# Performance work log

Hardware: AMD Instinct MI355X
Metric: run time of the kernel (lower is better)

The kernel has to match this reference:

```python
import jax, jax.numpy as jnp
import numpy as np

# Module hyperparameters (from init_kwargs)
B, C, T, H, W = 2, 128, 4, 64, 64
NHEADS = 32
SH, SW = 4, 4          # scales: patch size in H and W
GROUPS = C // 4        # GroupNorm groups = dim // 4
EPS = 1e-5


def _rel_index(t_, h_, w_):
    """(N,N) int32 index into the (2T-1)*(2h-1)*(2w-1) relative-position table."""
    tt = np.arange(t_); yy = np.arange(h_); xx = np.arange(w_)
    coords = np.stack(np.meshgrid(tt, yy, xx, indexing='ij'), -1).reshape(-1, 3)  # (N,3)
    rel = coords[:, None, :] - coords[None, :, :]                                 # (N,N,3)
    rel = rel + np.array([t_ - 1, h_ - 1, w_ - 1])
    idx = (rel[..., 0] * (2 * h_ - 1) + rel[..., 1]) * (2 * w_ - 1) + rel[..., 2]
    return idx.astype(np.int32)


def setup_inputs() -> dict:
    key = jax.random.key(0)
    ks = jax.random.split(key, 6)
    h, w = H // SH, W // SW
    table_sz = (2 * T - 1) * (2 * h - 1) * (2 * w - 1)
    inp = {
        "x": jax.random.normal(ks[0], (B, C, T, H, W), jnp.float32),
        "Wq": jax.random.normal(ks[1], (C, C), jnp.float32) / np.sqrt(C).astype(np.float32),
        "Wk": jax.random.normal(ks[2], (C, C), jnp.float32) / np.sqrt(C).astype(np.float32),
        "Wv": jax.random.normal(ks[3], (C, C), jnp.float32) / np.sqrt(C).astype(np.float32),
        "gq_gamma": jnp.ones((C,), jnp.float32), "gq_beta": jnp.zeros((C,), jnp.float32),
        "gk_gamma": jnp.ones((C,), jnp.float32), "gk_beta": jnp.zeros((C,), jnp.float32),
        "gv_gamma": jnp.ones((C,), jnp.float32), "gv_beta": jnp.zeros((C,), jnp.float32),
        "rel_table": jax.random.normal(ks[4], (NHEADS, table_sz), jnp.float32) * 0.02,
        "rel_index": jnp.asarray(_rel_index(T, h, w)),
    }
    return inp


def _group_norm(z, gamma, beta, groups, eps=EPS):
    b, c = z.shape[:2]
    zg = z.reshape(b, groups, c // groups, *z.shape[2:])
    mu = zg.mean(axis=(2, 3, 4, 5), keepdims=True)
    var = jnp.mean(jnp.square(zg - mu), axis=(2, 3, 4, 5), keepdims=True)
    zg = (zg - mu) * jax.lax.rsqrt(var + eps)
    zn = zg.reshape(z.shape)
    return zn * gamma[None, :, None, None, None] + beta[None, :, None, None, None]


def reference(x, Wq, Wk, Wv, gq_gamma, gq_beta, gk_gamma, gk_beta,
              gv_gamma, gv_beta, rel_table, rel_index):
    b, c, t, hh, ww = x.shape
    h, w = hh // SH, ww // SW
    n = t * h * w           # patch tokens
    p = SH * SW             # pixels per patch
    d = c // NHEADS         # head dim

    # 1x1x1 projections (pointwise conv == channel matmul) + GroupNorm
    q = _group_norm(jnp.einsum('bcthw,oc->bothw', x, Wq), gq_gamma, gq_beta, GROUPS)
    k = _group_norm(jnp.einsum('bcthw,oc->bothw', x, Wk), gk_gamma, gk_beta, GROUPS)
    v = _group_norm(jnp.einsum('bcthw,oc->bothw', x, Wv), gv_gamma, gv_beta, GROUPS)

    def to_patches(z):  # (b,c,t,H,W) -> (b,heads,d,N,P)
        z = z.reshape(b, NHEADS, d, t, h, SH, w, SW)
        z = z.transpose(0, 1, 2, 3, 4, 6, 5, 7)
        return z.reshape(b, NHEADS, d, n, p)

    qp = to_patches(q).mean(-1)     # pooled patch queries (b,g,d,N)
    kp = to_patches(k).mean(-1)     # pooled patch keys    (b,g,d,N)
    vp = to_patches(v)              # full-res values      (b,g,d,N,P)

    scale = 1.0 / jnp.sqrt(jnp.float32(d))
    logits = jnp.einsum('bgdn,bgdm->bgnm', qp, kp) * scale
    logits = logits + rel_table[:, rel_index][None]   # relative position bias (1,g,N,N)
    attn = jax.nn.softmax(logits, axis=-1)

    out = jnp.einsum('bgnm,bgdmp->bgdnp', attn, vp)   # (b,g,d,N,P)
    out = out.reshape(b, NHEADS, d, t, h, w, SH, SW).transpose(0, 1, 2, 3, 4, 6, 5, 7)
    out = out.reshape(b, c, t, hh, ww)                # (B,C,T,H,W) after outer permute
    return out
```

## Files before the change

### kernel.cpp

```cpp
#include <hip/hip_runtime.h>
#include <hip/hip_bf16.h>

#define B_ 2
#define C_ 128
#define G_ 32
#define N_ 1024
#define S_ 16384
#define TABLE_ 6727
#define EPS_ 1e-5f
#define LOG2E_ 1.44269504f
#define PSTB_ 64
#define NSTRIP_ 128

typedef __hip_bfloat16 bf16;
typedef __attribute__((ext_vector_type(8))) short short8;
typedef __attribute__((ext_vector_type(4))) float f32x4;

#if __has_builtin(__builtin_amdgcn_exp2f)
#define EXP2(x) __builtin_amdgcn_exp2f(x)
#else
#define EXP2(x) __expf((x) * 0.69314718056f)
#endif

__device__ __forceinline__ float bf2f(bf16 v) { return __bfloat162float(v); }
__device__ __forceinline__ float bits2f(unsigned u) { return __uint_as_float(u); }
__device__ __forceinline__ int dflag(const void* gq) {
  return (((const unsigned*)gq)[0] != 0x3F803F80u) ? 1 : 0;
}
__device__ __forceinline__ float ldcv(const void* p, int i, int fl) {
  return fl ? ((const float*)p)[i] : bf2f(((const bf16*)p)[i]);
}
__device__ __forceinline__ size_t spidx(int ttm, int b, int g) {
  return ((size_t)(((ttm * B_ + b) * G_) + g)) << 7;
}

__global__ __launch_bounds__(256) void proj_kernel(
    const void* __restrict__ x, const void* __restrict__ Wq,
    const void* __restrict__ Wk, const void* __restrict__ Wv,
    const void* __restrict__ gq,
    float* __restrict__ qpart, float* __restrict__ kpart,
    bf16* __restrict__ vpt, float* __restrict__ sp)
{
  __shared__ bf16 xs[128 * 128];
  __shared__ bf16 vs[8192];
  const int tid = threadIdx.x, lane = tid & 63, w = tid >> 6;
  const int s0 = blockIdx.x * 128;
  const int oh = blockIdx.y;
  const int b  = blockIdx.z;
  const int fl = dflag(gq);

  {
    const int s_lo = tid & 15, cb = tid >> 4;
    const size_t gc = (size_t)b * C_ * S_ + (size_t)(cb * 8) * S_ + s0 + s_lo;
#pragma unroll
    for (int i = 0; i < 8; ++i) {
      const int s = i * 16 + s_lo;
      union { short8 v; bf16 h[8]; } u;
      if (fl) {
#pragma unroll
        for (int j = 0; j < 8; ++j)
          u.h[j] = (bf16)((const float*)x)[gc + i * 16 + (size_t)j * S_];
      } else {
#pragma unroll
        for (int j = 0; j < 8; ++j)
          u.h[j] = ((const bf16*)x)[gc + i * 16 + (size_t)j * S_];
      }
      *(short8*)&xs[s * 128 + ((cb ^ (s & 7)) << 3)] = u.v;
    }
  }

  const int ow = oh * 4 + w;
  const int quad = lane >> 4;
  const int om = ow * 16 + (lane & 15);
  const void* const Ws[3] = {Wq, Wk, Wv};
  short8 afr[3][4];
#pragma unroll
  for (int tt = 0; tt < 3; ++tt)
#pragma unroll
    for (int kk = 0; kk < 4; ++kk) {
      const int off = om * 128 + kk * 32 + quad * 8;
      if (fl) {
        const float* wp = (const float*)Ws[tt] + off;
        const float4 a = *(const float4*)wp, bb = *(const float4*)(wp + 4);
        union { short8 s; bf16 h[8]; } u;
        u.h[0] = (bf16)a.x;  u.h[1] = (bf16)a.y;  u.h[2] = (bf16)a.z;  u.h[3] = (bf16)a.w;
        u.h[4] = (bf16)bb.x; u.h[5] = (bf16)bb.y; u.h[6] = (bf16)bb.z; u.h[7] = (bf16)bb.w;
        afr[tt][kk] = u.s;
      } else {
        afr[tt][kk] = *(const short8*)((const bf16*)Ws[tt] + off);
      }
    }
  __syncthreads();

  float ssum[3] = {0.f, 0.f, 0.f}, ssq[3] = {0.f, 0.f, 0.f};
  float psq[4][4] = {}, psk[4][4] = {};
  const int sl = lane & 15;
#pragma unroll
  for (int st = 0; st < 8; ++st) {
    f32x4 acc[3] = {{0,0,0,0},{0,0,0,0},{0,0,0,0}};
    const int srow = st * 16 + sl;
#pragma unroll
    for (int kk = 0; kk < 4; ++kk) {
      const short8 bv = *(const short8*)
          &xs[srow * 128 + ((((kk << 2) | quad) ^ (sl & 7)) << 3)];
      acc[0] = __builtin_amdgcn_mfma_f32_16x16x32_bf16(afr[0][kk], bv, acc[0], 0, 0, 0);
      acc[1] = __builtin_amdgcn_mfma_f32_16x16x32_bf16(afr[1][kk], bv, acc[1], 0, 0, 0);
      acc[2] = __builtin_amdgcn_mfma_f32_16x16x32_bf16(afr[2][kk], bv, acc[2], 0, 0, 0);
    }
    const int pIdx = (st >> 2) * 4 + (sl & 3);
    const int xp = (st & 3) * 4 + (sl >> 2);
#pragma unroll
    for (int r = 0; r < 4; ++r) {
      const float vq = acc[0][r], vk = acc[1][r], vv = acc[2][r];
      ssum[0] += vq; ssq[0] += vq * vq;
      ssum[1] += vk; ssq[1] += vk * vk;
      ssum[2] += vv; ssq[2] += vv * vv;
      float aq = vq + __shfl_xor(vq, 1); aq += __shfl_xor(aq, 2);
      float ak = vk + __shfl_xor(vk, 1); ak += __shfl_xor(ak, 2);
      psq[r][st & 3] += aq;
      psk[r][st & 3] += ak;
      const int o_loc = w * 16 + quad * 4 + r;
      vs[(o_loc * 8 + pIdx) * 16 + xp] = (bf16)vv;
    }
  }

  {
    const int c = sl & 3, wxl = sl >> 2;
    const int t = s0 >> 12;
    const int yy0 = (s0 >> 6) & 63;
    const int hy = yy0 >> 2, rp = (yy0 >> 1) & 1;
    const int nbase = t * 256 + hy * 16;
    const size_t pb = ((size_t)((b * 2 + rp) * C_ + ow * 16 + quad * 4 + c)) * N_ + nbase;
#pragma unroll
    for (int j = 0; j < 4; ++j) {
      float vq = psq[0][j];
      if (c == 1) vq = psq[1][j];
      if (c == 2) vq = psq[2][j];
      if (c == 3) vq = psq[3][j];
      float vk = psk[0][j];
      if (c == 1) vk = psk[1][j];
      if (c == 2) vk = psk[2][j];
      if (c == 3) vk = psk[3][j];
      qpart[pb + j * 4 + wxl] = vq;
      kpart[pb + j * 4 + wxl] = vk;
    }
  }

#pragma unroll
  for (int tt = 0; tt < 3; ++tt) {
#pragma unroll
    for (int off = 1; off < 16; off <<= 1) {
      ssum[tt] += __shfl_xor(ssum[tt], off);
      ssq[tt]  += __shfl_xor(ssq[tt], off);
    }
    if ((lane & 15) == 0) {
      const int grp = ow * 4 + quad;
      sp[spidx(tt * 2 + 0, b, grp) + blockIdx.x] = ssum[tt];
      sp[spidx(tt * 2 + 1, b, grp) + blockIdx.x] = ssq[tt];
    }
  }
  __syncthreads();

  const int rowp0 = (s0 >> 6) & 63;
  const int mIdx0 = (s0 >> 12) * 256 + (rowp0 >> 2) * 16;
  for (int cid = tid; cid < 1024; cid += 256) {
    const int half = cid & 1, run = cid >> 1;
    const int o_loc = run >> 3, pIdx = run & 7;
    const int o = oh * 64 + o_loc;
    const int gg = o >> 2, dd = o & 3;
    const int colv = dd * 16 + (rowp0 & 3) * 4 + pIdx;
    bf16* dst = vpt + ((size_t)(b * G_ + gg) * 64 + colv) * N_ + mIdx0 + half * 8;
    *(short8*)dst = *(const short8*)&vs[run * 16 + half * 8];
  }
}

__global__ __launch_bounds__(256, 4) void attn_kernel(
    const float* __restrict__ qpart, const float* __restrict__ kpart,
    const bf16* __restrict__ vpt, const void* __restrict__ rt,
    const void* __restrict__ gq, const void* __restrict__ bq,
    const void* __restrict__ gk, const void* __restrict__ bk,
    const void* __restrict__ gv, const void* __restrict__ bv,
    const float* __restrict__ sp, void* __restrict__ outv)
{
  const int g = blockIdx.y, b = blockIdx.z;
  const int tid = threadIdx.x, lane = tid & 63, w = tid >> 6;
  const int nw = blockIdx.x * 64;
  const int fl = dflag(gq);
  __shared__ __align__(16) char smem[37816];
  bf16* Vlds = (bf16*)smem;
  bf16* bldm = (bf16*)(smem + 8192);
  bf16* pldw = (bf16*)(smem + 13216) + w * 16 * PSTB_;
  bf16* klds = (bf16*)(smem + 21408);
  float* red = (float*)(smem + 37792);

  const int col = lane & 15, quad = lane >> 4;
  const size_t bg = (size_t)(b * G_ + g);
  const short* vpb = (const short*)vpt + bg * 64 * N_;
  const int vn0 = tid >> 3, kb8 = tid & 7;

  short8 st[2];
#pragma unroll
  for (int i = 0; i < 2; ++i)
    st[i] = *(const short8*)(vpb + (size_t)(i * 32 + vn0) * N_ + 0 * 64 + kb8 * 8);

  if (w < 2) {
#pragma unroll
    for (int j = 0; j < 3; ++j) {
      const float* a = sp + spidx(w + 2 * j, b, g);
      float v = a[lane] + a[lane + 64];
      v += __shfl_xor(v, 1);  v += __shfl_xor(v, 2);  v += __shfl_xor(v, 4);
      v += __shfl_xor(v, 8);  v += __shfl_xor(v, 16); v += __shfl_xor(v, 32);
      if (lane == 0) red[w + 2 * j] = v;
    }
  }

  const int tn = nw >> 8, yb = (nw >> 4) & 15;
  for (int i = tid; i < 2508; i += 256) {
    const int row = i / 33, d = i - row * 33;
    if (d < 31) {
      const int tm = row / 19, dyi = row - tm * 19;
      const int dt = tn - tm + 3;
      const int dy = yb + dyi;
      bldm[row * 33 + d] = (bf16)(ldcv(rt, g * TABLE_ + (dt * 31 + dy) * 31 + d, fl) * LOG2E_);
    }
  }
  __syncthreads();

  const float muq = red[0] * (1.f / 65536.f);
  const float rq = rsqrtf(red[1] * (1.f / 65536.f) - muq * muq + EPS_);
  const float muk = red[2] * (1.f / 65536.f);
  const float rk = rsqrtf(red[3] * (1.f / 65536.f) - muk * muk + EPS_);

  short8 af = {0, 0, 0, 0, 0, 0, 0, 0};
  if (quad < 2) {
    const int n = nw + w * 16 + col;
    union { short8 s; bf16 h[8]; } u;
#pragma unroll
    for (int d = 0; d < 4; ++d) {
      const int c = g * 4 + d;
      const float sq = qpart[((size_t)((b * 2 + 0) * C_ + c)) * N_ + n]
                     + qpart[((size_t)((b * 2 + 1) * C_ + c)) * N_ + n];
      const float qn = (sq * 0.0625f - muq) * rq * ldcv(gq, c, fl) + ldcv(bq, c, fl);
      const float qs = qn * (0.5f * LOG2E_);
      const bf16 qh = (bf16)qs;
      u.h[d] = qh; u.h[4 + d] = (bf16)(qs - bf2f(qh));
    }
    af = u.s;
  }

  {
    float gkv[4], bkv[4];
#pragma unroll
    for (int d = 0; d < 4; ++d) {
      gkv[d] = ldcv(gk, g * 4 + d, fl);
      bkv[d] = ldcv(bk, g * 4 + d, fl);
    }
#pragma unroll
    for (int i = 0; i < 4; ++i) {
      const int n = i * 256 + tid;
      union { short8 s; bf16 h[8]; } u;
#pragma unroll
      for (int d = 0; d < 4; ++d) {
        const int c = g * 4 + d;
        const float sk = kpart[((size_t)((b * 2 + 0) * C_ + c)) * N_ + n]
                       + kpart[((size_t)((b * 2 + 1) * C_ + c)) * N_ + n];
        const float kn = (sk * 0.0625f - muk) * rk * gkv[d] + bkv[d];
        const bf16 kh = (bf16)kn;
        u.h[d] = kh; u.h[4 + d] = (bf16)(kn - bf2f(kh));
      }
      *(short8*)&klds[n * 8] = u.s;
    }
  }
  __syncthreads();

  const short* klds_s = (const short*)klds;
  const short onebits = (short)0x3F80;
  const short8 ones8 = {onebits, onebits, onebits, onebits,
                        onebits, onebits, onebits, onebits};
  f32x4 acco[4] = {{0,0,0,0},{0,0,0,0},{0,0,0,0},{0,0,0,0}};
  f32x4 accs = {0.f, 0.f, 0.f, 0.f};

  ushort4 kv[4], kvn[4];
#pragma unroll
  for (int t = 0; t < 4; ++t)
    kv[t] = *(const ushort4*)(klds_s + ((0 * 4 + t) * 16 + col) * 8 + (quad & 1) * 4);

  for (int ch = 0; ch < 16; ++ch) {
    if (ch > 0) __syncthreads();
#pragma unroll
    for (int i = 0; i < 2; ++i) {
      const int n = i * 32 + vn0;
      *(short8*)&Vlds[n * 64 + ((kb8 ^ (n & 7)) << 3)] = st[i];
    }
    __syncthreads();
    if (ch < 15) {
#pragma unroll
      for (int i = 0; i < 2; ++i)
        st[i] = *(const short8*)(vpb + (size_t)(i * 32 + vn0) * N_ + (ch + 1) * 64 + kb8 * 8);
#pragma unroll
      for (int t = 0; t < 4; ++t)
        kvn[t] = *(const ushort4*)(klds_s + (((ch + 1) * 4 + t) * 16 + col) * 8 + (quad & 1) * 4);
    }
#pragma unroll
    for (int mt4 = 0; mt4 < 4; ++mt4) {
      const int mt = ch * 4 + mt4;
      const int tm = mt >> 4, ym = mt & 15;
      const short8 bf8 = {(short)kv[mt4].x, (short)kv[mt4].y, (short)kv[mt4].z, (short)kv[mt4].w,
                          (short)kv[mt4].x, (short)kv[mt4].y, (short)kv[mt4].z, (short)kv[mt4].w};
      f32x4 acc = {0.f, 0.f, 0.f, 0.f};
      acc = __builtin_amdgcn_mfma_f32_16x16x32_bf16(af, bf8, acc, 0, 0, 0);
      const int bbase = (tm * 19 + (w + 15 - ym)) * 33 + 15 + quad * 4 - col;
#pragma unroll
      for (int r = 0; r < 4; ++r) {
        const float e = EXP2(acc[r] + bf2f(bldm[bbase + r]));
        const int row = quad * 4 + r;
        pldw[row * PSTB_ + (((mt4 * 2 + (col >> 3)) ^ (row & 7)) << 3) + (col & 7)] = (bf16)e;
      }
    }
    __builtin_amdgcn_s_setprio(1);
#pragma unroll
    for (int ks = 0; ks < 2; ++ks) {
      const short8 a2 = *(const short8*)&pldw[col * PSTB_ + (((ks * 4 + quad) ^ (col & 7)) << 3)];
      accs = __builtin_amdgcn_mfma_f32_16x16x32_bf16(a2, ones8, accs, 0, 0, 0);
#pragma unroll
      for (int cc = 0; cc < 4; ++cc) {
        const int n = cc * 16 + col;
        const int kb = ks * 4 + quad;
        const short8 b2 = *(const short8*)&Vlds[n * 64 + ((kb ^ (n & 7)) << 3)];
        acco[cc] = __builtin_amdgcn_mfma_f32_16x16x32_bf16(a2, b2, acco[cc], 0, 0, 0);
      }
    }
    __builtin_amdgcn_s_setprio(0);
    if (ch < 15) {
#pragma unroll
      for (int t = 0; t < 4; ++t) kv[t] = kvn[t];
    }
  }

  __syncthreads();
  const float mu = red[4] * (1.f / 65536.f);
  const float rs = rsqrtf(red[5] * (1.f / 65536.f) - mu * mu + EPS_);
  const int sh = col >> 2, sw = col & 3;
  const size_t obase = (size_t)(b * C_ + g * 4) * S_ + tn * 4096 + (yb + w) * 256;
  if (!fl) {
    bf16* ost = (bf16*)(smem + w * 2048);
#pragma unroll
    for (int cc = 0; cc < 4; ++cc) {
      const int c = g * 4 + cc;
      const float alpha = rs * ldcv(gv, c, fl);
      const float beta = ldcv(bv, c, fl) - mu * alpha;
#pragma unroll
      for (int r = 0; r < 4; ++r) {
        const int xp = quad * 4 + r;
        ost[cc * 256 + sh * 64 + xp * 4 + sw] = (bf16)(alpha * (acco[cc][r] / accs[r]) + beta);
      }
    }
#pragma unroll
    for (int i = 0; i < 2; ++i) {
      const int e = (i * 64 + lane) * 8;
      const int cc = e >> 8, rem = e & 255;
      *(short8*)((bf16*)outv + obase + (size_t)cc * S_ + rem) = *(const short8*)&ost[e];
    }
  } else {
    float* ostf = (float*)smem + w * 1024;
#pragma unroll
    for (int cc = 0; cc < 4; ++cc) {
      const int c = g * 4 + cc;
      const float alpha = rs * ldcv(gv, c, fl);
      const float beta = ldcv(bv, c, fl) - mu * alpha;
#pragma unroll
      for (int r = 0; r < 4; ++r) {
        const int xp = quad * 4 + r;
        ostf[cc * 256 + sh * 64 + xp * 4 + sw] = alpha * (acco[cc][r] / accs[r]) + beta;
      }
    }
#pragma unroll
    for (int i = 0; i < 4; ++i) {
      const int e = (i * 64 + lane) * 4;
      const int cc = e >> 8, rem = e & 255;
      *(float4*)((float*)outv + obase + (size_t)cc * S_ + rem) = *(const float4*)&ostf[e];
    }
  }
}

extern "C" void kernel_launch(void* const* d_in, const int* in_sizes, int n_in,
                              void* d_out, int out_size, void* d_ws, size_t ws_size,
                              hipStream_t stream) {
  (void)in_sizes; (void)n_in; (void)out_size; (void)ws_size;
  const void* x  = d_in[0];
  const void* Wq = d_in[1];
  const void* Wk = d_in[2];
  const void* Wv = d_in[3];
  const void* gq = d_in[4];
  const void* bq = d_in[5];
  const void* gk = d_in[6];
  const void* bk = d_in[7];
  const void* gv = d_in[8];
  const void* bv = d_in[9];
  const void* rel_table = d_in[10];

  bf16*  vpt  = (bf16*)d_ws;
  float* qpart = (float*)(vpt + (size_t)B_ * G_ * 64 * N_);
  float* kpart = qpart + (size_t)B_ * 2 * C_ * N_;
  float* sp    = kpart + (size_t)B_ * 2 * C_ * N_;

  proj_kernel<<<dim3(NSTRIP_, 2, B_), 256, 0, stream>>>(
      x, Wq, Wk, Wv, gq, qpart, kpart, vpt, sp);
  attn_kernel<<<dim3(16, G_, B_), 256, 0, stream>>>(
      qpart, kpart, vpt, rel_table, gq, bq, gk, bk, gv, bv, sp, d_out);
}
```

Measured before the change: 158.8 us.

## Vectorize x loads with register transpose and make q/k partials channel-contiguous

The x staging in proj_kernel now loads 8 contiguous spatial elements per channel as vector loads. It transposes them in registers before writing to LDS, with a new XOR swizzle that the MFMA read side matches. The pooled q/k partial buffers move from channel-major to position-major with channels innermost, so attn_kernel can fetch a head's 4 channels with a single 16-byte load. This targets the uncoalesced scalar global loads in both kernels, at the cost of strided scattered writes of the partials and extra register shuffling.

```diff
diff --git a/kernel.cpp b/kernel.cpp
--- a/kernel.cpp
+++ b/kernel.cpp
@@ -50,22 +50,32 @@
   const int fl = dflag(gq);
 
   {
-    const int s_lo = tid & 15, cb = tid >> 4;
-    const size_t gc = (size_t)b * C_ * S_ + (size_t)(cb * 8) * S_ + s0 + s_lo;
-#pragma unroll
-    for (int i = 0; i < 8; ++i) {
-      const int s = i * 16 + s_lo;
-      union { short8 v; bf16 h[8]; } u;
-      if (fl) {
-#pragma unroll
-        for (int j = 0; j < 8; ++j)
-          u.h[j] = (bf16)((const float*)x)[gc + i * 16 + (size_t)j * S_];
-      } else {
-#pragma unroll
-        for (int j = 0; j < 8; ++j)
-          u.h[j] = ((const bf16*)x)[gc + i * 16 + (size_t)j * S_];
-      }
-      *(short8*)&xs[s * 128 + ((cb ^ (s & 7)) << 3)] = u.v;
+    const int cb = tid >> 4, sb = tid & 15;
+    const size_t gc0 = (size_t)b * C_ * S_ + (size_t)(cb * 8) * S_ + s0 + sb * 8;
+    union U8 { short8 v; ushort h[8]; };
+    U8 in[8];
+    if (fl) {
+#pragma unroll
+      for (int j = 0; j < 8; ++j) {
+        const float* xp = (const float*)x + gc0 + (size_t)j * S_;
+        const float4 a = *(const float4*)xp, b2 = *(const float4*)(xp + 4);
+        union { short8 s; bf16 hh[8]; } u;
+        u.hh[0] = (bf16)a.x;  u.hh[1] = (bf16)a.y;  u.hh[2] = (bf16)a.z;  u.hh[3] = (bf16)a.w;
+        u.hh[4] = (bf16)b2.x; u.hh[5] = (bf16)b2.y; u.hh[6] = (bf16)b2.z; u.hh[7] = (bf16)b2.w;
+        in[j].v = u.s;
+      }
+    } else {
+#pragma unroll
+      for (int j = 0; j < 8; ++j)
+        in[j].v = *(const short8*)((const bf16*)x + gc0 + (size_t)j * S_);
+    }
+#pragma unroll
+    for (int si = 0; si < 8; ++si) {
+      U8 o;
+#pragma unroll
+      for (int i = 0; i < 8; ++i) o.h[i] = in[i].h[si];
+      const int s = sb * 8 + si;
+      *(short8*)&xs[s * 128 + ((cb ^ si ^ (sb & 7)) << 3)] = o.v;
     }
   }
 
@@ -99,10 +109,11 @@
   for (int st = 0; st < 8; ++st) {
     f32x4 acc[3] = {{0,0,0,0},{0,0,0,0},{0,0,0,0}};
     const int srow = st * 16 + sl;
+    const int rxor = (sl & 7) ^ ((st << 1) & 7) ^ (sl >> 3);
 #pragma unroll
     for (int kk = 0; kk < 4; ++kk) {
       const short8 bv = *(const short8*)
-          &xs[srow * 128 + ((((kk << 2) | quad) ^ (sl & 7)) << 3)];
+          &xs[srow * 128 + ((((kk << 2) | quad) ^ rxor) << 3)];
       acc[0] = __builtin_amdgcn_mfma_f32_16x16x32_bf16(afr[0][kk], bv, acc[0], 0, 0, 0);
       acc[1] = __builtin_amdgcn_mfma_f32_16x16x32_bf16(afr[1][kk], bv, acc[1], 0, 0, 0);
       acc[2] = __builtin_amdgcn_mfma_f32_16x16x32_bf16(afr[2][kk], bv, acc[2], 0, 0, 0);
@@ -130,7 +141,7 @@
     const int yy0 = (s0 >> 6) & 63;
     const int hy = yy0 >> 2, rp = (yy0 >> 1) & 1;
     const int nbase = t * 256 + hy * 16;
-    const size_t pb = ((size_t)((b * 2 + rp) * C_ + ow * 16 + quad * 4 + c)) * N_ + nbase;
+    const size_t pb = ((size_t)(b * 2 + rp) * N_ + nbase) * C_ + ow * 16 + quad * 4 + c;
 #pragma unroll
     for (int j = 0; j < 4; ++j) {
       float vq = psq[0][j];
@@ -141,8 +152,8 @@
       if (c == 1) vk = psk[1][j];
       if (c == 2) vk = psk[2][j];
       if (c == 3) vk = psk[3][j];
-      qpart[pb + j * 4 + wxl] = vq;
-      kpart[pb + j * 4 + wxl] = vk;
+      qpart[pb + (size_t)(j * 4 + wxl) * C_] = vq;
+      kpart[pb + (size_t)(j * 4 + wxl) * C_] = vk;
     }
   }
 
@@ -234,12 +245,13 @@
   short8 af = {0, 0, 0, 0, 0, 0, 0, 0};
   if (quad < 2) {
     const int n = nw + w * 16 + col;
+    const f32x4 q0 = *(const f32x4*)&qpart[((size_t)(b * 2 + 0) * N_ + n) * C_ + g * 4];
+    const f32x4 q1 = *(const f32x4*)&qpart[((size_t)(b * 2 + 1) * N_ + n) * C_ + g * 4];
     union { short8 s; bf16 h[8]; } u;
 #pragma unroll
     for (int d = 0; d < 4; ++d) {
       const int c = g * 4 + d;
-      const float sq = qpart[((size_t)((b * 2 + 0) * C_ + c)) * N_ + n]
-                     + qpart[((size_t)((b * 2 + 1) * C_ + c)) * N_ + n];
+      const float sq = q0[d] + q1[d];
       const float qn = (sq * 0.0625f - muq) * rq * ldcv(gq, c, fl) + ldcv(bq, c, fl);
       const float qs = qn * (0.5f * LOG2E_);
       const bf16 qh = (bf16)qs;
@@ -258,13 +270,12 @@
 #pragma unroll
     for (int i = 0; i < 4; ++i) {
       const int n = i * 256 + tid;
+      const f32x4 k0 = *(const f32x4*)&kpart[((size_t)(b * 2 + 0) * N_ + n) * C_ + g * 4];
+      const f32x4 k1 = *(const f32x4*)&kpart[((size_t)(b * 2 + 1) * N_ + n) * C_ + g * 4];
       union { short8 s; bf16 h[8]; } u;
 #pragma unroll
       for (int d = 0; d < 4; ++d) {
-        const int c = g * 4 + d;
-        const float sk = kpart[((size_t)((b * 2 + 0) * C_ + c)) * N_ + n]
-                       + kpart[((size_t)((b * 2 + 1) * C_ + c)) * N_ + n];
-        const float kn = (sk * 0.0625f - muk) * rk * gkv[d] + bkv[d];
+        const float kn = ((k0[d] + k1[d]) * 0.0625f - muk) * rk * gkv[d] + bkv[d];
         const bf16 kh = (bf16)kn;
         u.h[d] = kh; u.h[4 + d] = (bf16)(kn - bf2f(kh));
       }
@@ -401,8 +412,8 @@
 
   bf16*  vpt  = (bf16*)d_ws;
   float* qpart = (float*)(vpt + (size_t)B_ * G_ * 64 * N_);
-  float* kpart = qpart + (size_t)B_ * 2 * C_ * N_;
-  float* sp    = kpart + (size_t)B_ * 2 * C_ * N_;
+  float* kpart = qpart + (size_t)B_ * 2 * N_ * C_;
+  float* sp    = kpart + (size_t)B_ * 2 * N_ * C_;
 
   proj_kernel<<<dim3(NSTRIP_, 2, B_), 256, 0, stream>>>(
       x, Wq, Wk, Wv, gq, qpart, kpart, vpt, sp);
```

After: 162.2 us. +2.2%, slower.
